# Kernel tuning notes

Measured on AMD Instinct MI355X. Metric: run time of the kernel, lower is better.

Reference implementation:

```python
import jax, jax.numpy as jnp
import numpy as np

B, S, C = 8, 1024, 768
H = 12            # num_heads
HD = C // H       # head_dim = 64
QH = QW = 32      # input_size; QH*QW == S


def setup_inputs() -> dict:
    key = jax.random.key(0)
    ks = jax.random.split(key, 6)
    return {
        "x": jax.random.normal(ks[0], (B, S, C), dtype=jnp.float32),
        "w_qkv": jax.random.normal(ks[1], (3 * C, C), dtype=jnp.float32) * 0.02,
        "w_out": jax.random.normal(ks[2], (C, C), dtype=jnp.float32) * 0.02,
        "b_out": jax.random.normal(ks[3], (C,), dtype=jnp.float32) * 0.02,
        "rel_pos_h": jax.random.normal(ks[4], (2 * QH - 1, HD), dtype=jnp.float32) * 0.02,
        "rel_pos_w": jax.random.normal(ks[5], (2 * QW - 1, HD), dtype=jnp.float32) * 0.02,
    }


def reference(x, w_qkv, w_out, b_out, rel_pos_h, rel_pos_w):
    scale = HD ** -0.5
    # qkv projection (no bias), rearrange 'b s (qkv h d) -> qkv b h s d'
    qkv = (x @ w_qkv.T).reshape(B, S, 3, H, HD).transpose(2, 0, 3, 1, 4)
    q, k, v = qkv[0], qkv[1], qkv[2]            # each (B, H, S, HD)

    attn = jnp.einsum('bhxd,bhyd->bhxy', q, k) * scale  # (B, H, S, S)

    # decomposed relative position bias (q_size == k_size, no interpolation)
    idx = jnp.arange(QH)[:, None] - jnp.arange(QH)[None, :] + (QH - 1)
    Rh = rel_pos_h[idx]                          # (QH, QH, HD)
    Rw = rel_pos_w[idx]                          # (QW, QW, HD)
    rq = q.reshape(B * H, QH, QW, HD)
    rel_h = jnp.einsum('bhwc,hkc->bhwk', rq, Rh)  # (BH, QH, QW, QH)
    rel_w = jnp.einsum('bhwc,wkc->bhwk', rq, Rw)  # (BH, QH, QW, QW)
    attn = (attn.reshape(B * H, QH, QW, QH, QW)
            + rel_h[:, :, :, :, None]
            + rel_w[:, :, :, None, :]).reshape(B, H, S, S)

    attn = jax.nn.softmax(attn, axis=-1)
    out = jnp.einsum('bhxy,bhyd->bhxd', attn, v)  # (B, H, S, HD)
    out = out.transpose(0, 2, 1, 3).reshape(B, S, C)
    return out @ w_out.T + b_out
```

## Files before the change

### kernel.cpp

```cpp
#include <hip/hip_runtime.h>
#include <cstdint>
#include <math.h>


using u16 = unsigned short;
using bf16x8 = __attribute__((ext_vector_type(8))) short;
using f32x4  = __attribute__((ext_vector_type(4))) float;

#define LOG2E 1.44269504088896340736f

__device__ __forceinline__ float bf2f(u16 u) {
  union { uint32_t i; float f; } v; v.i = ((uint32_t)u) << 16; return v.f;
}
__device__ __forceinline__ u16 f2bf(float f) {
  union { float f; uint32_t i; } v; v.f = f;
  uint32_t r = v.i + 0x7FFFu + ((v.i >> 16) & 1u);
  return (u16)(r >> 16);
}
__device__ __forceinline__ uint32_t cvt2(float a, float b) {
#if __has_builtin(__builtin_amdgcn_cvt_pk_bf16_f32)
  return __builtin_bit_cast(uint32_t, __builtin_amdgcn_cvt_pk_bf16_f32(a, b));
#else
  return (uint32_t)f2bf(a) | ((uint32_t)f2bf(b) << 16);
#endif
}
__device__ __forceinline__ float fexp2(float x) {
#if __has_builtin(__builtin_amdgcn_exp2f)
  return __builtin_amdgcn_exp2f(x);
#else
  return exp2f(x);
#endif
}
__device__ __forceinline__ uint4 pack8(float4 a, float4 b) {
  uint4 r;
  r.x = cvt2(a.x, a.y); r.y = cvt2(a.z, a.w);
  r.z = cvt2(b.x, b.y); r.w = cvt2(b.z, b.w);
  return r;
}
union U4BF8 { uint4 u; bf16x8 v; };

__device__ __forceinline__ void load16_to_lds(const void* g, void* l) {
  auto gp = reinterpret_cast<const __attribute__((address_space(1))) uint32_t*>(
      reinterpret_cast<uintptr_t>(g));
  auto lp = reinterpret_cast<__attribute__((address_space(3))) uint32_t*>(
      reinterpret_cast<uintptr_t>(l));
  __builtin_amdgcn_global_load_lds(gp, lp, 16, 0, 0);
}

__global__ __launch_bounds__(256, 8)
void cvt_bf16(const float* __restrict__ s0, u16* __restrict__ d0, int n0,
              const float* __restrict__ s1, u16* __restrict__ d1, int n1,
              const float* __restrict__ s2, u16* __restrict__ d2)
{
  int i = (blockIdx.x*256 + threadIdx.x) * 8;
  const float* s; u16* d; int off;
  if (i < n0)            { s = s0; d = d0; off = i; }
  else if (i < n0 + n1)  { s = s1; d = d1; off = i - n0; }
  else                   { s = s2; d = d2; off = i - n0 - n1; }
  float4 a = *(const float4*)(s + off);
  float4 b = *(const float4*)(s + off + 4);
  *(uint4*)(d + off) = pack8(a, b);
}

__global__ __launch_bounds__(256, 2)
void qkv_gemm(const u16* __restrict__ xb, const u16* __restrict__ wqb,
              u16* __restrict__ Q, u16* __restrict__ K, u16* __restrict__ VT)
{
  __shared__ u16 sA[256*64];
  __shared__ u16 sB[128*64];
  const int tid  = threadIdx.x;
  const int lane = tid & 63, wid = tid >> 6;
  const int quad = lane >> 4, l16 = lane & 15;
  const int blk = blockIdx.x;
  const int tn = (blk >> 3) % 18;
  const int tm = (blk & 7) + (blk / 144) * 8;
  const int wm = wid & 1, wn = wid >> 1;

  const u16* gA[8]; const u16* gB[4];
  #pragma unroll
  for (int it = 0; it < 8; ++it) {
    int g = it*256 + tid;
    int row = g >> 3;
    int cg  = (g & 7) ^ (row & 7);
    gA[it] = xb  + (size_t)(tm*256 + row)*768 + cg*8;
  }
  #pragma unroll
  for (int it = 0; it < 4; ++it) {
    int g = it*256 + tid;
    int row = g >> 3;
    int cg  = (g & 7) ^ (row & 7);
    gB[it] = wqb + (size_t)(tn*128 + row)*768 + cg*8;
  }

  const f32x4 fz = {0.f, 0.f, 0.f, 0.f};
  f32x4 acc[8][4];
  #pragma unroll
  for (int i = 0; i < 8; ++i)
    #pragma unroll
    for (int j = 0; j < 4; ++j) acc[i][j] = fz;

  for (int k0 = 0; k0 < 768; k0 += 64) {
    #pragma unroll
    for (int it = 0; it < 8; ++it)
      load16_to_lds(gA[it] + k0, (char*)sA + (it*256 + tid)*16);
    #pragma unroll
    for (int it = 0; it < 4; ++it)
      load16_to_lds(gB[it] + k0, (char*)sB + (it*256 + tid)*16);
    __syncthreads();
    #pragma unroll
    for (int ks = 0; ks < 2; ++ks) {
      bf16x8 bfv[4];
      #pragma unroll
      for (int nt = 0; nt < 4; ++nt) {
        int n = wn*64 + nt*16 + l16;
        bfv[nt] = *(const bf16x8*)&sB[(n*8 + ((ks*4 + quad) ^ (n & 7)))*8];
      }
      #pragma unroll
      for (int mt = 0; mt < 8; ++mt) {
        int m = wm*128 + mt*16 + l16;
        bf16x8 af = *(const bf16x8*)&sA[(m*8 + ((ks*4 + quad) ^ (m & 7)))*8];
        #pragma unroll
        for (int nt = 0; nt < 4; ++nt)
          acc[mt][nt] = __builtin_amdgcn_mfma_f32_16x16x32_bf16(af, bfv[nt], acc[mt][nt], 0, 0, 0);
      }
    }
    __syncthreads();
  }

  const float KSCL = 0.125f * LOG2E;
  #pragma unroll
  for (int mt = 0; mt < 8; ++mt) {
    #pragma unroll
    for (int nt = 0; nt < 4; ++nt) {
      const int col = wn*64 + nt*16 + l16;
      const int n = tn*128 + col;
      #pragma unroll
      for (int r = 0; r < 4; ++r) {
        const int rowin = wm*128 + mt*16 + quad*4 + r;
        const int m = tm*256 + rowin;
        const int b = m >> 10, s = m & 1023;
        if (n < 768) {
          int h = n >> 6, d = n & 63;
          Q[(((size_t)b*12 + h)*1024 + s)*64 + d] = f2bf(acc[mt][nt][r]);
        } else if (n < 1536) {
          int nn = n - 768; int h = nn >> 6, d = nn & 63;
          int bh = b*12 + h;
          int kb = s >> 7, srel = s & 127;
          K[(size_t)bh*65536
            + (((kb*8 + (srel >> 4))*2 + (d >> 5))*4 + ((d >> 3) & 3))*128
            + (srel & 15)*8 + (d & 7)] = f2bf(acc[mt][nt][r] * KSCL);
        } else {
          int nn = n - 1536; int h = nn >> 6, d = nn & 63;
          int bh = b*12 + h;
          int kb = s >> 7, srel = s & 127;
          VT[(size_t)bh*65536
             + ((((kb*2 + (srel >> 6))*2 + ((srel >> 5) & 1))*4 + (d >> 4))*4 + ((srel >> 3) & 3))*128
             + (d & 15)*8 + (srel & 7)] = f2bf(acc[mt][nt][r]);
        }
      }
    }
  }
}

__global__ __launch_bounds__(256, 4)
void rel_bias(const u16* __restrict__ Q, const float* __restrict__ rph, const float* __restrict__ rpw,
              u16* __restrict__ RH, u16* __restrict__ RW)
{
  const int tid  = threadIdx.x;
  const int lane = tid & 63, wid = tid >> 6;
  const int quad = lane >> 4, l16 = lane & 15;
  const int blk = blockIdx.x;
  const int gx = (blk >> 3) & 7;
  const int bh = (blk & 7) + (blk >> 6) * 8;
  const bool isW = gx >= 4;
  const float* rp = isW ? rpw : rph;
  u16* RO = isW ? RW : RH;
  const int qb = (gx & 3)*8 + wid*2;
  const f32x4 fz = {0.f, 0.f, 0.f, 0.f};

  #pragma unroll
  for (int gi = 0; gi < 2; ++gi) {
    const int qv = qb + gi;
    f32x4 acc[2][2];
    #pragma unroll
    for (int i = 0; i < 2; ++i)
      #pragma unroll
      for (int j = 0; j < 2; ++j) acc[i][j] = fz;

    #pragma unroll
    for (int ks = 0; ks < 2; ++ks) {
      bf16x8 af[2], bfv[2];
      #pragma unroll
      for (int mt = 0; mt < 2; ++mt) {
        int m = mt*16 + l16;
        int xrow = isW ? (m*32 + qv) : (qv*32 + m);
        af[mt] = *(const bf16x8*)(Q + ((size_t)bh*1024 + xrow)*64 + ks*32 + quad*8);
      }
      #pragma unroll
      for (int nt = 0; nt < 2; ++nt) {
        int n = nt*16 + l16;
        const float* bp = rp + (size_t)(qv - n + 31)*64 + ks*32 + quad*8;
        U4BF8 c; c.u = pack8(*(const float4*)bp, *(const float4*)(bp + 4));
        bfv[nt] = c.v;
      }
      #pragma unroll
      for (int mt = 0; mt < 2; ++mt)
        #pragma unroll
        for (int nt = 0; nt < 2; ++nt)
          acc[mt][nt] = __builtin_amdgcn_mfma_f32_16x16x32_bf16(af[mt], bfv[nt], acc[mt][nt], 0, 0, 0);
    }
    #pragma unroll
    for (int mt = 0; mt < 2; ++mt)
      #pragma unroll
      for (int nt = 0; nt < 2; ++nt)
        #pragma unroll
        for (int r = 0; r < 4; ++r) {
          int j = mt*16 + quad*4 + r;
          int xrow = isW ? (j*32 + qv) : (qv*32 + j);
          int n = nt*16 + l16;
          RO[((size_t)bh*1024 + xrow)*32 + n] = f2bf(acc[mt][nt][r] * LOG2E);
        }
  }
}

__global__ __launch_bounds__(512, 4)
void attn_kernel(const u16* __restrict__ Q, const u16* __restrict__ KF, const u16* __restrict__ VF,
                 const u16* __restrict__ RH, const u16* __restrict__ RW, u16* __restrict__ AO)
{
  __shared__ u16 sK[2][8192];
  __shared__ u16 sV[2][8192];
  __shared__ u16 sP[128*64];
  const int tid  = threadIdx.x;
  const int lane = tid & 63, wid = tid >> 6;
  const int quad = lane >> 4, l16 = lane & 15;
  const int blk = blockIdx.x;
  const int qt = (blk >> 3) & 7;
  const int bh = (blk & 7) + (blk >> 6) * 8;
  const int q0 = qt * 128;
  const int ql = wid*16 + l16;

  bf16x8 qf[2];
  #pragma unroll
  for (int ks = 0; ks < 2; ++ks)
    qf[ks] = *(const bf16x8*)(Q + ((size_t)bh*1024 + q0 + ql)*64 + ks*32 + quad*8);

  const size_t ro = ((size_t)bh*1024 + q0 + ql)*32;
  float bwv[2][4];
  #pragma unroll
  for (int h2 = 0; h2 < 2; ++h2) {
    uint2 t = *(const uint2*)(RW + ro + h2*16 + quad*4);
    bwv[h2][0] = bf2f((u16)(t.x & 0xFFFF));
    bwv[h2][1] = bf2f((u16)(t.x >> 16));
    bwv[h2][2] = bf2f((u16)(t.y & 0xFFFF));
    bwv[h2][3] = bf2f((u16)(t.y >> 16));
  }

  const u16* KFs = KF + (size_t)bh*65536;
  const u16* VFs = VF + (size_t)bh*65536;

  load16_to_lds(KFs + tid*8,        (char*)&sK[0][0] + tid*16);
  load16_to_lds(KFs + 4096 + tid*8, (char*)&sK[0][0] + 8192 + tid*16);
  load16_to_lds(VFs + tid*8,        (char*)&sV[0][0] + tid*16);
  load16_to_lds(VFs + 4096 + tid*8, (char*)&sV[0][0] + 8192 + tid*16);

  const f32x4 fz = {0.f, 0.f, 0.f, 0.f};
  f32x4 lsv = fz;
  f32x4 accO[4];
  #pragma unroll
  for (int dt = 0; dt < 4; ++dt) accO[dt] = fz;

  int cur = 0;
  for (int kb = 0; kb < 8; ++kb) {
    uint2 bhl = *(const uint2*)(RH + ro + kb*4);

    if (kb < 7) {
      const u16* ks = KFs + (size_t)(kb + 1)*8192;
      const u16* vs = VFs + (size_t)(kb + 1)*8192;
      char* dk = (char*)&sK[cur ^ 1][0];
      char* dv = (char*)&sV[cur ^ 1][0];
      __builtin_amdgcn_sched_barrier(0);
      load16_to_lds(ks + tid*8,        dk + tid*16);
      load16_to_lds(ks + 4096 + tid*8, dk + 8192 + tid*16);
      load16_to_lds(vs + tid*8,        dv + tid*16);
      load16_to_lds(vs + 4096 + tid*8, dv + 8192 + tid*16);
      __builtin_amdgcn_sched_barrier(0);
      asm volatile("s_waitcnt vmcnt(4)" ::: "memory");
    } else {
      asm volatile("s_waitcnt vmcnt(0)" ::: "memory");
    }
    __builtin_amdgcn_s_barrier();
    __builtin_amdgcn_sched_barrier(0);

    const u16* sKc = &sK[cur][0];
    const u16* sVc = &sV[cur][0];

    #pragma unroll
    for (int h = 0; h < 2; ++h) {
      f32x4 sAcc[4];
      #pragma unroll
      for (int smt = 0; smt < 4; ++smt) {
        const int g = h*2 + (smt >> 1);
        const uint32_t gw = (g < 2) ? bhl.x : bhl.y;
        const float bhf = bf2f((u16)(gw >> ((g & 1)*16)));
        #pragma unroll
        for (int r = 0; r < 4; ++r) sAcc[smt][r] = bhf + bwv[smt & 1][r];
      }
      __builtin_amdgcn_s_setprio(1);
      #pragma unroll
      for (int ks = 0; ks < 2; ++ks) {
        #pragma unroll
        for (int smt = 0; smt < 4; ++smt) {
          bf16x8 af = *(const bf16x8*)&sKc[(size_t)(((h*4 + smt)*2 + ks))*512 + lane*8];
          sAcc[smt] = __builtin_amdgcn_mfma_f32_16x16x32_bf16(af, qf[ks], sAcc[smt], 0, 0, 0);
        }
      }
      __builtin_amdgcn_s_setprio(0);

      #pragma unroll
      for (int smt = 0; smt < 4; ++smt) {
        #pragma unroll
        for (int r = 0; r < 4; ++r) {
          float p = fexp2(sAcc[smt][r]);
          sAcc[smt][r] = p;
          lsv[r] += p;
        }
      }

      #pragma unroll
      for (int smt = 0; smt < 4; ++smt) {
        uint2 w;
        w.x = cvt2(sAcc[smt][0], sAcc[smt][1]);
        w.y = cvt2(sAcc[smt][2], sAcc[smt][3]);
        const int sg = smt*2 + (quad >> 1);
        *(uint2*)&sP[ql*64 + ((sg ^ (ql & 7))*8) + (quad & 1)*4] = w;
      }

      #pragma unroll
      for (int ka = 0; ka < 2; ++ka) {
        bf16x8 pf = *(const bf16x8*)&sP[ql*64 + (((ka*4 + quad) ^ (ql & 7))*8)];
        __builtin_amdgcn_s_setprio(1);
        #pragma unroll
        for (int dt = 0; dt < 4; ++dt) {
          bf16x8 vf = *(const bf16x8*)&sVc[(size_t)(((h*2 + ka)*4 + dt))*512 + lane*8];
          accO[dt] = __builtin_amdgcn_mfma_f32_16x16x32_bf16(vf, pf, accO[dt], 0, 0, 0);
        }
        __builtin_amdgcn_s_setprio(0);
      }
    }

    __builtin_amdgcn_sched_barrier(0);
    __builtin_amdgcn_s_barrier();
    __builtin_amdgcn_sched_barrier(0);
    cur ^= 1;
  }

  const int b = bh / 12, head = bh % 12;
  float s = lsv[0] + lsv[1] + lsv[2] + lsv[3];
  s += __shfl_xor(s, 16);
  s += __shfl_xor(s, 32);
  const float inv = 1.f / s;
  const size_t base = ((size_t)(b*1024 + q0 + ql))*768 + head*64;
  #pragma unroll
  for (int dt = 0; dt < 4; ++dt) {
    uint2 o;
    o.x = cvt2(accO[dt][0]*inv, accO[dt][1]*inv);
    o.y = cvt2(accO[dt][2]*inv, accO[dt][3]*inv);
    *(uint2*)&AO[base + dt*16 + quad*4] = o;
  }
}

__global__ __launch_bounds__(256, 4)
void out_gemm(const u16* __restrict__ A, const u16* __restrict__ wob, const float* __restrict__ bout,
              float* __restrict__ out)
{
  __shared__ u16 sA[128*64];
  __shared__ u16 sB[128*64];
  const int tid  = threadIdx.x;
  const int lane = tid & 63, wid = tid >> 6;
  const int quad = lane >> 4, l16 = lane & 15;
  const int blk = blockIdx.x;
  const int tn = (blk >> 3) % 6;
  const int tm = (blk & 7) + (blk / 48) * 8;
  const int wm = wid & 1, wn = wid >> 1;

  const u16* gA[4]; const u16* gB[4];
  #pragma unroll
  for (int it = 0; it < 4; ++it) {
    int g = it*256 + tid;
    int row = g >> 3;
    int cg  = (g & 7) ^ (row & 7);
    gA[it] = A   + (size_t)(tm*128 + row)*768 + cg*8;
    gB[it] = wob + (size_t)(tn*128 + row)*768 + cg*8;
  }

  const f32x4 fz = {0.f, 0.f, 0.f, 0.f};
  f32x4 acc[4][4];
  #pragma unroll
  for (int i = 0; i < 4; ++i)
    #pragma unroll
    for (int j = 0; j < 4; ++j) acc[i][j] = fz;

  for (int k0 = 0; k0 < 768; k0 += 64) {
    #pragma unroll
    for (int it = 0; it < 4; ++it) {
      int g = it*256 + tid;
      load16_to_lds(gA[it] + k0, (char*)sA + g*16);
      load16_to_lds(gB[it] + k0, (char*)sB + g*16);
    }
    __syncthreads();
    #pragma unroll
    for (int ks = 0; ks < 2; ++ks) {
      bf16x8 af[4], bfv[4];
      #pragma unroll
      for (int mt = 0; mt < 4; ++mt) {
        int m = wm*64 + mt*16 + l16;
        af[mt] = *(const bf16x8*)&sA[(m*8 + ((ks*4 + quad) ^ (m & 7)))*8];
      }
      #pragma unroll
      for (int nt = 0; nt < 4; ++nt) {
        int n = wn*64 + nt*16 + l16;
        bfv[nt] = *(const bf16x8*)&sB[(n*8 + ((ks*4 + quad) ^ (n & 7)))*8];
      }
      #pragma unroll
      for (int mt = 0; mt < 4; ++mt)
        #pragma unroll
        for (int nt = 0; nt < 4; ++nt)
          acc[mt][nt] = __builtin_amdgcn_mfma_f32_16x16x32_bf16(af[mt], bfv[nt], acc[mt][nt], 0, 0, 0);
    }
    __syncthreads();
  }

  #pragma unroll
  for (int mt = 0; mt < 4; ++mt) {
    #pragma unroll
    for (int nt = 0; nt < 4; ++nt) {
      const int n = tn*128 + wn*64 + nt*16 + l16;
      const float bv = bout[n];
      #pragma unroll
      for (int r = 0; r < 4; ++r) {
        const int rowin = wm*64 + mt*16 + quad*4 + r;
        out[(size_t)(tm*128 + rowin)*768 + n] = acc[mt][nt][r] + bv;
      }
    }
  }
}

extern "C" void kernel_launch(void* const* d_in, const int* in_sizes, int n_in,
                              void* d_out, int out_size, void* d_ws, size_t ws_size,
                              hipStream_t stream)
{
  const float* x    = (const float*)d_in[0];
  const float* wqkv = (const float*)d_in[1];
  const float* wout = (const float*)d_in[2];
  const float* bout = (const float*)d_in[3];
  const float* rph  = (const float*)d_in[4];
  const float* rpw  = (const float*)d_in[5];
  float* out = (float*)d_out;

  char* ws = (char*)d_ws;
  const size_t SZ = (size_t)96*1024*64;
  u16* Q   = (u16*)ws;
  u16* K   = Q  + SZ;
  u16* VT  = K  + SZ;
  u16* RH  = VT + SZ;
  u16* RW  = RH + (size_t)96*1024*32;
  u16* AO  = RW + (size_t)96*1024*32;
  u16* xb  = AO + SZ;
  u16* wqb = xb + SZ;
  u16* wob = wqb + (size_t)2304*768;

  const int n0 = 8192*768, n1 = 2304*768;
  cvt_bf16   <<<dim3(4224), dim3(256), 0, stream>>>(x, xb, n0, wqkv, wqb, n1, wout, wob);
  qkv_gemm   <<<dim3(576),  dim3(256), 0, stream>>>(xb, wqb, Q, K, VT);
  rel_bias   <<<dim3(768),  dim3(256), 0, stream>>>(Q, rph, rpw, RH, RW);
  attn_kernel<<<dim3(768),  dim3(512), 0, stream>>>(Q, K, VT, RH, RW, AO);
  out_gemm   <<<dim3(384),  dim3(256), 0, stream>>>(AO, wob, bout, out);
}
```

Measured before the change: 225.1 us.

## Double-buffer LDS tiles in QKV and output GEMMs with async prefetch

Both projection GEMMs now use two LDS buffers with a K-step of 32 instead of one buffer with a K-step of 64. The next tile's global-to-LDS loads are issued before computing on the current tile, using explicit vmcnt waits and barriers so memory latency overlaps MFMA work. The LDS swizzle is adapted to the 4-chunk row layout, and setprio raises wave priority during the MFMA block. The halved K-step doubles the number of barriers per GEMM, and the hand-counted vmcnt values must match the number of loads in flight.

```diff
diff --git a/kernel.cpp b/kernel.cpp
--- a/kernel.cpp
+++ b/kernel.cpp
@@ -66,8 +66,8 @@
 void qkv_gemm(const u16* __restrict__ xb, const u16* __restrict__ wqb,
               u16* __restrict__ Q, u16* __restrict__ K, u16* __restrict__ VT)
 {
-  __shared__ u16 sA[256*64];
-  __shared__ u16 sB[128*64];
+  __shared__ u16 sA[2][256*32];
+  __shared__ u16 sB[2][128*32];
   const int tid  = threadIdx.x;
   const int lane = tid & 63, wid = tid >> 6;
   const int quad = lane >> 4, l16 = lane & 15;
@@ -76,19 +76,19 @@
   const int tm = (blk & 7) + (blk / 144) * 8;
   const int wm = wid & 1, wn = wid >> 1;
 
-  const u16* gA[8]; const u16* gB[4];
-  #pragma unroll
-  for (int it = 0; it < 8; ++it) {
-    int g = it*256 + tid;
-    int row = g >> 3;
-    int cg  = (g & 7) ^ (row & 7);
-    gA[it] = xb  + (size_t)(tm*256 + row)*768 + cg*8;
-  }
+  const u16* gA[4]; const u16* gB[2];
   #pragma unroll
   for (int it = 0; it < 4; ++it) {
     int g = it*256 + tid;
-    int row = g >> 3;
-    int cg  = (g & 7) ^ (row & 7);
+    int row = g >> 2;
+    int cg  = (g & 3) ^ ((row >> 1) & 3);
+    gA[it] = xb  + (size_t)(tm*256 + row)*768 + cg*8;
+  }
+  #pragma unroll
+  for (int it = 0; it < 2; ++it) {
+    int g = it*256 + tid;
+    int row = g >> 2;
+    int cg  = (g & 3) ^ ((row >> 1) & 3);
     gB[it] = wqb + (size_t)(tn*128 + row)*768 + cg*8;
   }
 
@@ -99,32 +99,56 @@
     #pragma unroll
     for (int j = 0; j < 4; ++j) acc[i][j] = fz;
 
-  for (int k0 = 0; k0 < 768; k0 += 64) {
-    #pragma unroll
-    for (int it = 0; it < 8; ++it)
-      load16_to_lds(gA[it] + k0, (char*)sA + (it*256 + tid)*16);
-    #pragma unroll
-    for (int it = 0; it < 4; ++it)
-      load16_to_lds(gB[it] + k0, (char*)sB + (it*256 + tid)*16);
-    __syncthreads();
-    #pragma unroll
-    for (int ks = 0; ks < 2; ++ks) {
-      bf16x8 bfv[4];
-      #pragma unroll
-      for (int nt = 0; nt < 4; ++nt) {
-        int n = wn*64 + nt*16 + l16;
-        bfv[nt] = *(const bf16x8*)&sB[(n*8 + ((ks*4 + quad) ^ (n & 7)))*8];
-      }
-      #pragma unroll
-      for (int mt = 0; mt < 8; ++mt) {
-        int m = wm*128 + mt*16 + l16;
-        bf16x8 af = *(const bf16x8*)&sA[(m*8 + ((ks*4 + quad) ^ (m & 7)))*8];
-        #pragma unroll
-        for (int nt = 0; nt < 4; ++nt)
-          acc[mt][nt] = __builtin_amdgcn_mfma_f32_16x16x32_bf16(af, bfv[nt], acc[mt][nt], 0, 0, 0);
-      }
-    }
-    __syncthreads();
+  #pragma unroll
+  for (int it = 0; it < 4; ++it)
+    load16_to_lds(gA[it], (char*)&sA[0][0] + (it*256 + tid)*16);
+  #pragma unroll
+  for (int it = 0; it < 2; ++it)
+    load16_to_lds(gB[it], (char*)&sB[0][0] + (it*256 + tid)*16);
+
+  int cur = 0;
+  for (int k = 0; k < 24; ++k) {
+    if (k < 23) {
+      const int k0 = (k + 1)*32;
+      char* dA = (char*)&sA[cur ^ 1][0];
+      char* dB = (char*)&sB[cur ^ 1][0];
+      __builtin_amdgcn_sched_barrier(0);
+      #pragma unroll
+      for (int it = 0; it < 4; ++it)
+        load16_to_lds(gA[it] + k0, dA + (it*256 + tid)*16);
+      #pragma unroll
+      for (int it = 0; it < 2; ++it)
+        load16_to_lds(gB[it] + k0, dB + (it*256 + tid)*16);
+      __builtin_amdgcn_sched_barrier(0);
+      asm volatile("s_waitcnt vmcnt(6)" ::: "memory");
+    } else {
+      asm volatile("s_waitcnt vmcnt(0)" ::: "memory");
+    }
+    __builtin_amdgcn_s_barrier();
+    __builtin_amdgcn_sched_barrier(0);
+
+    const u16* sAc = &sA[cur][0];
+    const u16* sBc = &sB[cur][0];
+    bf16x8 bfv[4];
+    #pragma unroll
+    for (int nt = 0; nt < 4; ++nt) {
+      int n = wn*64 + nt*16 + l16;
+      bfv[nt] = *(const bf16x8*)&sBc[(n*4 + (quad ^ ((n >> 1) & 3)))*8];
+    }
+    __builtin_amdgcn_s_setprio(1);
+    #pragma unroll
+    for (int mt = 0; mt < 8; ++mt) {
+      int m = wm*128 + mt*16 + l16;
+      bf16x8 af = *(const bf16x8*)&sAc[(m*4 + (quad ^ ((m >> 1) & 3)))*8];
+      #pragma unroll
+      for (int nt = 0; nt < 4; ++nt)
+        acc[mt][nt] = __builtin_amdgcn_mfma_f32_16x16x32_bf16(af, bfv[nt], acc[mt][nt], 0, 0, 0);
+    }
+    __builtin_amdgcn_s_setprio(0);
+    __builtin_amdgcn_sched_barrier(0);
+    __builtin_amdgcn_s_barrier();
+    __builtin_amdgcn_sched_barrier(0);
+    cur ^= 1;
   }
 
   const float KSCL = 0.125f * LOG2E;
@@ -373,8 +397,8 @@
 void out_gemm(const u16* __restrict__ A, const u16* __restrict__ wob, const float* __restrict__ bout,
               float* __restrict__ out)
 {
-  __shared__ u16 sA[128*64];
-  __shared__ u16 sB[128*64];
+  __shared__ u16 sA[2][128*32];
+  __shared__ u16 sB[2][128*32];
   const int tid  = threadIdx.x;
   const int lane = tid & 63, wid = tid >> 6;
   const int quad = lane >> 4, l16 = lane & 15;
@@ -383,12 +407,12 @@
   const int tm = (blk & 7) + (blk / 48) * 8;
   const int wm = wid & 1, wn = wid >> 1;
 
-  const u16* gA[4]; const u16* gB[4];
-  #pragma unroll
-  for (int it = 0; it < 4; ++it) {
+  const u16* gA[2]; const u16* gB[2];
+  #pragma unroll
+  for (int it = 0; it < 2; ++it) {
     int g = it*256 + tid;
-    int row = g >> 3;
-    int cg  = (g & 7) ^ (row & 7);
+    int row = g >> 2;
+    int cg  = (g & 3) ^ ((row >> 1) & 3);
     gA[it] = A   + (size_t)(tm*128 + row)*768 + cg*8;
     gB[it] = wob + (size_t)(tn*128 + row)*768 + cg*8;
   }
@@ -400,34 +424,56 @@
     #pragma unroll
     for (int j = 0; j < 4; ++j) acc[i][j] = fz;
 
-  for (int k0 = 0; k0 < 768; k0 += 64) {
-    #pragma unroll
-    for (int it = 0; it < 4; ++it) {
-      int g = it*256 + tid;
-      load16_to_lds(gA[it] + k0, (char*)sA + g*16);
-      load16_to_lds(gB[it] + k0, (char*)sB + g*16);
-    }
-    __syncthreads();
-    #pragma unroll
-    for (int ks = 0; ks < 2; ++ks) {
-      bf16x8 af[4], bfv[4];
-      #pragma unroll
-      for (int mt = 0; mt < 4; ++mt) {
-        int m = wm*64 + mt*16 + l16;
-        af[mt] = *(const bf16x8*)&sA[(m*8 + ((ks*4 + quad) ^ (m & 7)))*8];
-      }
-      #pragma unroll
-      for (int nt = 0; nt < 4; ++nt) {
-        int n = wn*64 + nt*16 + l16;
-        bfv[nt] = *(const bf16x8*)&sB[(n*8 + ((ks*4 + quad) ^ (n & 7)))*8];
-      }
-      #pragma unroll
-      for (int mt = 0; mt < 4; ++mt)
-        #pragma unroll
-        for (int nt = 0; nt < 4; ++nt)
-          acc[mt][nt] = __builtin_amdgcn_mfma_f32_16x16x32_bf16(af[mt], bfv[nt], acc[mt][nt], 0, 0, 0);
-    }
-    __syncthreads();
+  #pragma unroll
+  for (int it = 0; it < 2; ++it) {
+    load16_to_lds(gA[it], (char*)&sA[0][0] + (it*256 + tid)*16);
+    load16_to_lds(gB[it], (char*)&sB[0][0] + (it*256 + tid)*16);
+  }
+
+  int cur = 0;
+  for (int k = 0; k < 24; ++k) {
+    if (k < 23) {
+      const int k0 = (k + 1)*32;
+      char* dA = (char*)&sA[cur ^ 1][0];
+      char* dB = (char*)&sB[cur ^ 1][0];
+      __builtin_amdgcn_sched_barrier(0);
+      #pragma unroll
+      for (int it = 0; it < 2; ++it) {
+        load16_to_lds(gA[it] + k0, dA + (it*256 + tid)*16);
+        load16_to_lds(gB[it] + k0, dB + (it*256 + tid)*16);
+      }
+      __builtin_amdgcn_sched_barrier(0);
+      asm volatile("s_waitcnt vmcnt(4)" ::: "memory");
+    } else {
+      asm volatile("s_waitcnt vmcnt(0)" ::: "memory");
+    }
+    __builtin_amdgcn_s_barrier();
+    __builtin_amdgcn_sched_barrier(0);
+
+    const u16* sAc = &sA[cur][0];
+    const u16* sBc = &sB[cur][0];
+    bf16x8 af[4], bfv[4];
+    #pragma unroll
+    for (int mt = 0; mt < 4; ++mt) {
+      int m = wm*64 + mt*16 + l16;
+      af[mt] = *(const bf16x8*)&sAc[(m*4 + (quad ^ ((m >> 1) & 3)))*8];
+    }
+    #pragma unroll
+    for (int nt = 0; nt < 4; ++nt) {
+      int n = wn*64 + nt*16 + l16;
+      bfv[nt] = *(const bf16x8*)&sBc[(n*4 + (quad ^ ((n >> 1) & 3)))*8];
+    }
+    __builtin_amdgcn_s_setprio(1);
+    #pragma unroll
+    for (int mt = 0; mt < 4; ++mt)
+      #pragma unroll
+      for (int nt = 0; nt < 4; ++nt)
+        acc[mt][nt] = __builtin_amdgcn_mfma_f32_16x16x32_bf16(af[mt], bfv[nt], acc[mt][nt], 0, 0, 0);
+    __builtin_amdgcn_s_setprio(0);
+    __builtin_amdgcn_sched_barrier(0);
+    __builtin_amdgcn_s_barrier();
+    __builtin_amdgcn_sched_barrier(0);
+    cur ^= 1;
   }
 
   #pragma unroll
```

New measurement: 211.4 us. 1.06x faster.
